# Performance work log

Measured on AMD Instinct MI355X. Metric: run time of the kernel, lower is better.

Reference implementation:

```python
import jax, jax.numpy as jnp
import numpy as np
import math

D_MODEL = 512
D_STATE = 16
D_CONV = 4
EXPAND = 2
D_INNER = EXPAND * D_MODEL          # 1024
D_HALF = D_INNER // 2               # 512
DT_RANK = math.ceil(D_MODEL / 16)   # 32
BATCH, SEQLEN = 2, 4096
DT_MIN, DT_MAX, DT_FLOOR = 0.001, 0.1, 1e-4


def setup_inputs() -> dict:
    key = jax.random.key(0)
    ks = jax.random.split(key, 9)

    def lin(k, fan_out, fan_in):
        return jax.random.normal(k, (fan_out, fan_in), jnp.float32) / np.float32(np.sqrt(fan_in))

    hidden_states = jax.random.normal(ks[0], (BATCH, SEQLEN, D_MODEL), jnp.float32)
    in_proj_w = lin(ks[1], D_INNER, D_MODEL)
    x_proj_w = lin(ks[2], DT_RANK + 2 * D_STATE, D_HALF)
    dt_std = np.float32(DT_RANK ** -0.5)
    dt_proj_w = jax.random.uniform(ks[3], (D_HALF, DT_RANK), jnp.float32, -dt_std, dt_std)
    dt = jnp.exp(jax.random.uniform(ks[4], (D_HALF,), jnp.float32)
                 * (math.log(DT_MAX) - math.log(DT_MIN)) + math.log(DT_MIN))
    dt = jnp.clip(dt, DT_FLOOR)
    dt_proj_b = dt + jnp.log(-jnp.expm1(-dt))  # inverse-softplus init
    A_log = jnp.log(jnp.tile(jnp.arange(1, D_STATE + 1, dtype=jnp.float32)[None, :], (D_HALF, 1)))
    D = jnp.ones((D_HALF,), jnp.float32)
    out_proj_w = lin(ks[5], D_MODEL, D_INNER)
    conv1d_x_w = jax.random.normal(ks[6], (D_HALF, 1, D_CONV), jnp.float32) / np.float32(np.sqrt(D_CONV))
    conv1d_z_w = jax.random.normal(ks[7], (D_HALF, 1, D_CONV), jnp.float32) / np.float32(np.sqrt(D_CONV))
    return dict(hidden_states=hidden_states, in_proj_w=in_proj_w,
                conv1d_x_w=conv1d_x_w, conv1d_z_w=conv1d_z_w,
                x_proj_w=x_proj_w, dt_proj_w=dt_proj_w, dt_proj_b=dt_proj_b,
                A_log=A_log, D=D, out_proj_w=out_proj_w)


def _dwconv_same(x, w):
    # x: (b, c, l); w: (c, 1, k) depthwise. torch padding='same' with k=4 pads (1, 2),
    # which matches lax 'SAME'.
    return jax.lax.conv_general_dilated(
        x, w, window_strides=(1,), padding='SAME',
        dimension_numbers=('NCH', 'OIH', 'NCH'),
        feature_group_count=x.shape[1])


def _selective_scan(x, delta, A, B, C, D):
    # x, delta: (b, d, l); A: (d, n); B, C: (b, n, l); D: (d,)
    dA = jnp.exp(jnp.einsum('bdl,dn->bldn', delta, A))        # (b, l, d, n)
    dBx = jnp.einsum('bdl,bnl,bdl->bldn', delta, B, x)        # (b, l, d, n)

    def combine(c1, c2):
        a1, b1 = c1
        a2, b2 = c2
        return a1 * a2, a2 * b1 + b2

    _, h = jax.lax.associative_scan(combine, (dA, dBx), axis=1)  # h: (b, l, d, n)
    y = jnp.einsum('bldn,bnl->bdl', h, C) + D[None, :, None] * x
    return y


def reference(hidden_states, in_proj_w, conv1d_x_w, conv1d_z_w, x_proj_w,
              dt_proj_w, dt_proj_b, A_log, D, out_proj_w):
    b, l, _ = hidden_states.shape
    xz = jnp.einsum('bld,ed->bel', hidden_states, in_proj_w)   # (b, d_inner, l)
    x, z = jnp.split(xz, 2, axis=1)                            # each (b, d_half, l)
    A = -jnp.exp(A_log.astype(jnp.float32))
    x = jax.nn.silu(_dwconv_same(x, conv1d_x_w))
    z = jax.nn.silu(_dwconv_same(z, conv1d_z_w))
    x_dbl = jnp.einsum('bdl,ed->bel', x, x_proj_w)             # (b, dt_rank+2n, l)
    dt_r = x_dbl[:, :DT_RANK]                                  # (b, dt_rank, l)
    Bm = x_dbl[:, DT_RANK:DT_RANK + D_STATE]                   # (b, n, l)
    Cm = x_dbl[:, DT_RANK + D_STATE:]                          # (b, n, l)
    dt = jnp.einsum('brl,dr->bdl', dt_r, dt_proj_w)            # (b, d_half, l)
    delta = jax.nn.softplus(dt + dt_proj_b.astype(jnp.float32)[None, :, None])
    y = _selective_scan(x, delta, A, Bm, Cm, D.astype(jnp.float32))
    y = jnp.concatenate([y, z], axis=1)                        # (b, d_inner, l)
    out = jnp.einsum('bdl,ed->ble', y, out_proj_w)             # (b, l, d_model)
    return out
```

## Files before the change

kernel.cpp:

```cpp
#include <hip/hip_runtime.h>
#include <math.h>

#define BB 2
#define LL 4096
#define DMODEL 512
#define DINNER 1024
#define DHALF 512
#define DSTATE 16
#define RK 32
#define NCH 64
#define NC 128
#define CLEN (LL/NC)
#define NG 16
#define GL (NC/NG)

typedef __attribute__((ext_vector_type(8))) short short8;
typedef __attribute__((ext_vector_type(4))) float f32x4;

__device__ __forceinline__ float silu_f(float v) { return v / (1.f + __expf(-v)); }

__device__ __forceinline__ unsigned short f2bf(float x) {
    unsigned int u = __float_as_uint(x);
    u += 0x7fffu + ((u >> 16) & 1u);
    return (unsigned short)(u >> 16);
}
__device__ __forceinline__ float bf2f(unsigned short u) {
    return __uint_as_float((unsigned int)u << 16);
}

__device__ __forceinline__ float softplus_f(float x) {
    return fmaxf(x, 0.f) + __logf(1.f + __expf(-fabsf(x)));
}

__device__ __forceinline__ void gload16(const unsigned short* g, unsigned short* l) {
    __builtin_amdgcn_global_load_lds((const __attribute__((address_space(1))) void*)g,
                                     (__attribute__((address_space(3))) void*)l, 16, 0, 0);
}

#define H4  1048576
#define W14 131072
#define W24 131072
#define W34 8192
__global__ void cast_all(const float* __restrict__ hid, const float* __restrict__ w1,
                         const float* __restrict__ w2, const float* __restrict__ w3,
                         unsigned short* __restrict__ Hb, unsigned short* __restrict__ Wb,
                         unsigned short* __restrict__ Wob, unsigned short* __restrict__ Wxb) {
    int i = blockIdx.x * 256 + threadIdx.x;
    const float* src; unsigned short* dst; int j;
    if (i < H4)                    { src = hid; dst = Hb;  j = i; }
    else if (i < H4 + W14)         { src = w1;  dst = Wb;  j = i - H4; }
    else if (i < H4 + W14 + W24)   { src = w2;  dst = Wob; j = i - H4 - W14; }
    else if (i < H4 + W14 + W24 + W34) { src = w3; dst = Wxb; j = i - H4 - W14 - W24; }
    else return;
    float4 v = *(const float4*)&src[(size_t)j * 4];
    ushort4 o = make_ushort4(f2bf(v.x), f2bf(v.y), f2bf(v.z), f2bf(v.w));
    *(ushort4*)&dst[(size_t)j * 4] = o;
}

template<int K, int E, bool BF16OUT>
__global__ __launch_bounds__(256) void gemm_mfma(const unsigned short* __restrict__ W,
                                                 const unsigned short* __restrict__ X,
                                                 void* __restrict__ outv) {
    __shared__ unsigned short Wa[128 * 64];
    __shared__ unsigned short Xa[128 * 64];
    const int tid = threadIdx.x;
    const int lane = tid & 63;
    const int w = tid >> 6;
    const int wr = w >> 1, wc = w & 1;
    const int frow = lane & 15;
    const int kg = lane >> 4;
    const int e0 = blockIdx.y * 128;
    const int r0 = blockIdx.x * 128;

    f32x4 acc[4][4] = {};

    for (int kt = 0; kt < K / 64; ++kt) {
        #pragma unroll
        for (int i = 0; i < 4; ++i) {
            int flat = i * 256 + tid;
            int row = flat >> 3;
            int slot = flat & 7;
            int chunk = slot ^ (row & 7);
            gload16(&W[(size_t)(e0 + row) * K + kt * 64 + chunk * 8], &Wa[flat * 8]);
            gload16(&X[(size_t)(r0 + row) * K + kt * 64 + chunk * 8], &Xa[flat * 8]);
        }
        __syncthreads();

        #pragma unroll
        for (int ks = 0; ks < 2; ++ks) {
            short8 af[4], bfr[4];
            #pragma unroll
            for (int m = 0; m < 4; ++m) {
                int row = wr * 64 + m * 16 + frow;
                int phys = (ks * 4 + kg) ^ (row & 7);
                af[m] = *(const short8*)&Wa[row * 64 + phys * 8];
            }
            #pragma unroll
            for (int n = 0; n < 4; ++n) {
                int row = wc * 64 + n * 16 + frow;
                int phys = (ks * 4 + kg) ^ (row & 7);
                bfr[n] = *(const short8*)&Xa[row * 64 + phys * 8];
            }
            #pragma unroll
            for (int m = 0; m < 4; ++m)
                #pragma unroll
                for (int n = 0; n < 4; ++n)
                    acc[m][n] = __builtin_amdgcn_mfma_f32_16x16x32_bf16(af[m], bfr[n], acc[m][n], 0, 0, 0);
        }
        __syncthreads();
    }

    #pragma unroll
    for (int m = 0; m < 4; ++m) {
        #pragma unroll
        for (int n = 0; n < 4; ++n) {
            int e = e0 + wr * 64 + m * 16 + kg * 4;
            int r = r0 + wc * 64 + n * 16 + frow;
            f32x4 a = acc[m][n];
            if constexpr (BF16OUT) {
                ushort4 o = make_ushort4(f2bf(a.x), f2bf(a.y), f2bf(a.z), f2bf(a.w));
                *(ushort4*)&((unsigned short*)outv)[(size_t)r * E + e] = o;
            } else {
                *(f32x4*)&((float*)outv)[(size_t)r * E + e] = a;
            }
        }
    }
}

__global__ __launch_bounds__(256) void gemm_xproj(const unsigned short* __restrict__ W,
                                                  const unsigned short* __restrict__ X,
                                                  float* __restrict__ out) {
    __shared__ unsigned short Xa[128 * 64];
    __shared__ unsigned short Wa[64 * 64];
    const int tid = threadIdx.x;
    const int lane = tid & 63;
    const int w = tid >> 6;
    const int frow = lane & 15;
    const int kg = lane >> 4;
    const int r0 = blockIdx.x * 128;

    f32x4 acc[4][2] = {};

    for (int kt = 0; kt < 512 / 64; ++kt) {
        #pragma unroll
        for (int i = 0; i < 4; ++i) {
            int flat = i * 256 + tid;
            int row = flat >> 3;
            int slot = flat & 7;
            int chunk = slot ^ (row & 7);
            gload16(&X[(size_t)(r0 + row) * 512 + kt * 64 + chunk * 8], &Xa[flat * 8]);
        }
        #pragma unroll
        for (int i = 0; i < 2; ++i) {
            int flat = i * 256 + tid;
            int row = flat >> 3;
            int slot = flat & 7;
            int chunk = slot ^ (row & 7);
            gload16(&W[(size_t)row * 512 + kt * 64 + chunk * 8], &Wa[flat * 8]);
        }
        __syncthreads();

        #pragma unroll
        for (int ks = 0; ks < 2; ++ks) {
            short8 af[4], bfr[2];
            #pragma unroll
            for (int m = 0; m < 4; ++m) {
                int row = m * 16 + frow;
                int phys = (ks * 4 + kg) ^ (row & 7);
                af[m] = *(const short8*)&Wa[row * 64 + phys * 8];
            }
            #pragma unroll
            for (int n = 0; n < 2; ++n) {
                int row = w * 32 + n * 16 + frow;
                int phys = (ks * 4 + kg) ^ (row & 7);
                bfr[n] = *(const short8*)&Xa[row * 64 + phys * 8];
            }
            #pragma unroll
            for (int m = 0; m < 4; ++m)
                #pragma unroll
                for (int n = 0; n < 2; ++n)
                    acc[m][n] = __builtin_amdgcn_mfma_f32_16x16x32_bf16(af[m], bfr[n], acc[m][n], 0, 0, 0);
        }
        __syncthreads();
    }

    #pragma unroll
    for (int m = 0; m < 4; ++m) {
        #pragma unroll
        for (int n = 0; n < 2; ++n) {
            int r = r0 + w * 32 + n * 16 + frow;
            int b = r >> 12;
            int l = r & (LL - 1);
            int e = m * 16 + kg * 4;
            #pragma unroll
            for (int i = 0; i < 4; ++i)
                out[((size_t)b * NCH + e + i) * LL + l] = acc[m][n][i];
        }
    }
}

__global__ void conv_silu(const unsigned short* __restrict__ xzb,
                          const float* __restrict__ wx, const float* __restrict__ wz,
                          unsigned short* __restrict__ xqb, unsigned short* __restrict__ ycb) {
    __shared__ float s[67][64];
    const int b = blockIdx.z;
    const int l0 = blockIdx.x * 64;
    const int c0 = blockIdx.y * 64;
    const int tid = threadIdx.x;
    for (int idx = tid; idx < 67 * 16; idx += 256) {
        int rr = idx >> 4, u = idx & 15;
        int l = l0 - 1 + rr;
        float4 f;
        if (l >= 0 && l < LL) {
            ushort4 v = *(const ushort4*)&xzb[((size_t)b * LL + l) * DINNER + c0 + u * 4];
            f = make_float4(bf2f(v.x), bf2f(v.y), bf2f(v.z), bf2f(v.w));
        } else f = make_float4(0.f, 0.f, 0.f, 0.f);
        *(float4*)&s[rr][u * 4] = f;
    }
    __syncthreads();
    const int ct = (tid & 15) * 4;
    const int c = c0 + ct;
    const bool isx = (c < DHALF);
    const float* wp = isx ? &wx[c * 4] : &wz[(c - DHALF) * 4];
    float4 w0 = *(const float4*)&wp[0];
    float4 w1 = *(const float4*)&wp[4];
    float4 w2 = *(const float4*)&wp[8];
    float4 w3 = *(const float4*)&wp[12];
    #pragma unroll
    for (int rep = 0; rep < 4; ++rep) {
        int ll = (tid >> 4) + rep * 16;
        float4 t0 = *(const float4*)&s[ll][ct];
        float4 t1 = *(const float4*)&s[ll + 1][ct];
        float4 t2 = *(const float4*)&s[ll + 2][ct];
        float4 t3 = *(const float4*)&s[ll + 3][ct];
        float v0 = w0.x*t0.x + w0.y*t1.x + w0.z*t2.x + w0.w*t3.x;
        float v1 = w1.x*t0.y + w1.y*t1.y + w1.z*t2.y + w1.w*t3.y;
        float v2 = w2.x*t0.z + w2.y*t1.z + w2.z*t2.z + w2.w*t3.z;
        float v3 = w3.x*t0.w + w3.y*t1.w + w3.z*t2.w + w3.w*t3.w;
        ushort4 o = make_ushort4(f2bf(silu_f(v0)), f2bf(silu_f(v1)),
                                 f2bf(silu_f(v2)), f2bf(silu_f(v3)));
        int l = l0 + ll;
        if (isx) *(ushort4*)&xqb[((size_t)b * LL + l) * DHALF + c] = o;
        else     *(ushort4*)&ycb[((size_t)b * LL + l) * DINNER + c] = o;
    }
}

__global__ __launch_bounds__(256) void scan1(const unsigned short* __restrict__ xqb,
                      const float* __restrict__ xdbl, const float* __restrict__ A_log,
                      const float* __restrict__ dtw, const float* __restrict__ dtb,
                      float* __restrict__ pend, float* __restrict__ hend) {
    __shared__ float s[48][CLEN];
    const int b = blockIdx.z;
    const int d = blockIdx.y * 256 + threadIdx.x;
    const int c = blockIdx.x;
    const int tid = threadIdx.x;
    for (int idx = tid; idx < 48 * CLEN; idx += 256) {
        int ch = idx / CLEN, ll = idx % CLEN;
        s[ch][ll] = xdbl[((size_t)b * NCH + ch) * LL + c * CLEN + ll];
    }
    float dtwreg[RK];
    #pragma unroll
    for (int r = 0; r < RK; r += 4) {
        float4 v = *(const float4*)&dtw[d * RK + r];
        dtwreg[r] = v.x; dtwreg[r+1] = v.y; dtwreg[r+2] = v.z; dtwreg[r+3] = v.w;
    }
    float Arow[DSTATE];
    #pragma unroll
    for (int n = 0; n < DSTATE; ++n) Arow[n] = -expf(A_log[d * DSTATE + n]);
    const float bias = dtb[d];
    float del[CLEN];
    #pragma unroll
    for (int t = 0; t < CLEN; ++t) del[t] = bias;
    __syncthreads();
    #pragma unroll
    for (int r = 0; r < RK; ++r) {
        float wv = dtwreg[r];
        #pragma unroll
        for (int q = 0; q < CLEN / 4; ++q) {
            float4 v = *(const float4*)&s[r][q * 4];
            del[q*4+0] = fmaf(v.x, wv, del[q*4+0]);
            del[q*4+1] = fmaf(v.y, wv, del[q*4+1]);
            del[q*4+2] = fmaf(v.z, wv, del[q*4+2]);
            del[q*4+3] = fmaf(v.w, wv, del[q*4+3]);
        }
    }
    #pragma unroll
    for (int t = 0; t < CLEN; ++t) del[t] = softplus_f(del[t]);

    float h[DSTATE], p[DSTATE];
    #pragma unroll
    for (int n = 0; n < DSTATE; ++n) { h[n] = 0.f; p[n] = 1.f; }
    #pragma unroll
    for (int t = 0; t < CLEN; ++t) {
        float dl = del[t];
        float xv = bf2f(xqb[((size_t)b * LL + c * CLEN + t) * DHALF + d]);
        float dx = dl * xv;
        #pragma unroll
        for (int n = 0; n < DSTATE; ++n) {
            float dA = __expf(dl * Arow[n]);
            h[n] = fmaf(dA, h[n], dx * s[32 + n][t]);
            p[n] *= dA;
        }
    }
    size_t base = (((size_t)b * NC + c) * DSTATE) * DHALF + d;
    #pragma unroll
    for (int n = 0; n < DSTATE; ++n) {
        pend[base + (size_t)n * DHALF] = p[n];
        hend[base + (size_t)n * DHALF] = h[n];
    }
}

__global__ void scan2a(float* __restrict__ pend, float* __restrict__ hend,
                       float* __restrict__ gP, float* __restrict__ gH) {
    int flat = blockIdx.x * 256 + threadIdx.x;
    int d = flat & (DHALF - 1);
    int n = (flat >> 9) & (DSTATE - 1);
    int g = (flat >> 13) & (NG - 1);
    int b = flat >> 17;
    const size_t stride = (size_t)DSTATE * DHALF;
    size_t idx = (((size_t)b * NC + g * GL) * DSTATE + n) * DHALF + d;
    float P = 1.f, H = 0.f;
    #pragma unroll
    for (int j = 0; j < GL; ++j) {
        float p = pend[idx], h = hend[idx];
        pend[idx] = P; hend[idx] = H;
        H = fmaf(p, H, h);
        P *= p;
        idx += stride;
    }
    size_t gi = (((size_t)b * NG + g) * DSTATE + n) * DHALF + d;
    gP[gi] = P; gH[gi] = H;
}

__global__ void scan2b(const float* __restrict__ gP, float* __restrict__ gH) {
    int flat = blockIdx.x * 256 + threadIdx.x;
    int d = flat & (DHALF - 1);
    int n = (flat >> 9) & (DSTATE - 1);
    int b = flat >> 13;
    float h = 0.f;
    const size_t stride = (size_t)DSTATE * DHALF;
    size_t gi = (((size_t)b * NG) * DSTATE + n) * DHALF + d;
    for (int g = 0; g < NG; ++g) {
        float P = gP[gi], Hh = gH[gi];
        gH[gi] = h;
        h = fmaf(P, h, Hh);
        gi += stride;
    }
}

__global__ __launch_bounds__(256) void scan3(const unsigned short* __restrict__ xqb,
                      const float* __restrict__ xdbl, const float* __restrict__ A_log,
                      const float* __restrict__ dtw, const float* __restrict__ dtb,
                      const float* __restrict__ Dp, const float* __restrict__ pend,
                      const float* __restrict__ hend, const float* __restrict__ gH,
                      unsigned short* __restrict__ ycb) {
    __shared__ float s[64][CLEN];
    const int b = blockIdx.z;
    const int d = blockIdx.y * 256 + threadIdx.x;
    const int c = blockIdx.x;
    const int tid = threadIdx.x;
    for (int idx = tid; idx < 64 * CLEN; idx += 256) {
        int ch = idx / CLEN, ll = idx % CLEN;
        s[ch][ll] = xdbl[((size_t)b * NCH + ch) * LL + c * CLEN + ll];
    }
    float dtwreg[RK];
    #pragma unroll
    for (int r = 0; r < RK; r += 4) {
        float4 v = *(const float4*)&dtw[d * RK + r];
        dtwreg[r] = v.x; dtwreg[r+1] = v.y; dtwreg[r+2] = v.z; dtwreg[r+3] = v.w;
    }
    float Arow[DSTATE], h[DSTATE];
    size_t base = (((size_t)b * NC + c) * DSTATE) * DHALF + d;
    size_t gbase = (((size_t)b * NG + (c / GL)) * DSTATE) * DHALF + d;
    #pragma unroll
    for (int n = 0; n < DSTATE; ++n) {
        Arow[n] = -expf(A_log[d * DSTATE + n]);
        h[n] = fmaf(pend[base + (size_t)n * DHALF], gH[gbase + (size_t)n * DHALF],
                    hend[base + (size_t)n * DHALF]);
    }
    const float bias = dtb[d];
    const float Dv = Dp[d];
    float del[CLEN];
    #pragma unroll
    for (int t = 0; t < CLEN; ++t) del[t] = bias;
    __syncthreads();
    #pragma unroll
    for (int r = 0; r < RK; ++r) {
        float wv = dtwreg[r];
        #pragma unroll
        for (int q = 0; q < CLEN / 4; ++q) {
            float4 v = *(const float4*)&s[r][q * 4];
            del[q*4+0] = fmaf(v.x, wv, del[q*4+0]);
            del[q*4+1] = fmaf(v.y, wv, del[q*4+1]);
            del[q*4+2] = fmaf(v.z, wv, del[q*4+2]);
            del[q*4+3] = fmaf(v.w, wv, del[q*4+3]);
        }
    }
    #pragma unroll
    for (int t = 0; t < CLEN; ++t) del[t] = softplus_f(del[t]);

    #pragma unroll
    for (int t = 0; t < CLEN; ++t) {
        float dl = del[t];
        float xv = bf2f(xqb[((size_t)b * LL + c * CLEN + t) * DHALF + d]);
        float dx = dl * xv;
        float y = Dv * xv;
        #pragma unroll
        for (int n = 0; n < DSTATE; ++n) {
            float dA = __expf(dl * Arow[n]);
            h[n] = fmaf(dA, h[n], dx * s[32 + n][t]);
            y = fmaf(h[n], s[48 + n][t], y);
        }
        ycb[((size_t)b * LL + c * CLEN + t) * DINNER + d] = f2bf(y);
    }
}

extern "C" void kernel_launch(void* const* d_in, const int* in_sizes, int n_in,
                              void* d_out, int out_size, void* d_ws, size_t ws_size,
                              hipStream_t stream) {
    const float* hidden     = (const float*)d_in[0];
    const float* in_proj_w  = (const float*)d_in[1];
    const float* conv_x_w   = (const float*)d_in[2];
    const float* conv_z_w   = (const float*)d_in[3];
    const float* x_proj_w   = (const float*)d_in[4];
    const float* dt_proj_w  = (const float*)d_in[5];
    const float* dt_proj_b  = (const float*)d_in[6];
    const float* A_log      = (const float*)d_in[7];
    const float* Dp         = (const float*)d_in[8];
    const float* out_proj_w = (const float*)d_in[9];
    float* out = (float*)d_out;

    float* ws_f = (float*)d_ws;
    unsigned short* Wb  = (unsigned short*)(ws_f + 0);
    unsigned short* Wob = (unsigned short*)(ws_f + 262144);
    unsigned short* Wxb = (unsigned short*)(ws_f + 524288);
    unsigned short* Hb  = (unsigned short*)(ws_f + 540672);
    unsigned short* xzb = (unsigned short*)(ws_f + 2637824);
    unsigned short* xqb = (unsigned short*)(ws_f + 6832128);
    unsigned short* ycb = (unsigned short*)(ws_f + 8929280);
    float* xdbl = ws_f + 13123584;
    float* gP   = ws_f + 13647872;
    float* gH   = ws_f + 13910016;
    float* pend = ws_f + 2637824;
    float* hend = ws_f + 540672;

    dim3 blk(256);

    cast_all<<<dim3((H4 + W14 + W24 + W34 + 255) / 256), blk, 0, stream>>>(
        hidden, in_proj_w, out_proj_w, x_proj_w, Hb, Wb, Wob, Wxb);
    gemm_mfma<DMODEL, DINNER, true><<<dim3(BB * LL / 128, DINNER / 128), blk, 0, stream>>>(Wb, Hb, xzb);
    conv_silu<<<dim3(LL / 64, DINNER / 64, BB), blk, 0, stream>>>(xzb, conv_x_w, conv_z_w, xqb, ycb);
    gemm_xproj<<<dim3(BB * LL / 128), blk, 0, stream>>>(Wxb, xqb, xdbl);
    scan1<<<dim3(NC, DHALF / 256, BB), blk, 0, stream>>>(xqb, xdbl, A_log, dt_proj_w, dt_proj_b, pend, hend);
    scan2a<<<dim3(BB * NG * DSTATE * DHALF / 256), blk, 0, stream>>>(pend, hend, gP, gH);
    scan2b<<<dim3(BB * DSTATE * DHALF / 256), blk, 0, stream>>>(gP, gH);
    scan3<<<dim3(NC, DHALF / 256, BB), blk, 0, stream>>>(xqb, xdbl, A_log, dt_proj_w, dt_proj_b,
                                                         Dp, pend, hend, gH, ycb);
    gemm_mfma<DINNER, DMODEL, false><<<dim3(BB * LL / 128, DMODEL / 128), blk, 0, stream>>>(Wob, ycb, out);
}
```

Baseline: 134.8 us.

## Use exp2 with prescaled A, closed-form chunk decay, and XCD-aware GEMM tile remap

The scan kernels now fold log2(e) into A so each decay factor is a single exp2 instead of exp with an extra multiply. The first scan pass no longer multiplies a running product per state; it sums the deltas and computes the chunk decay once as exp2(A*sum(delta)). The GEMM kernel remaps block IDs so consecutive blocks on the same XCD share weight tiles, which targets L2 locality. The closed-form product changes rounding slightly, and the remap assumes gridDim.x is divisible by 8.

Measured after the change: 157.5 us. 16.9% more time.

```diff
diff --git a/kernel.cpp b/kernel.cpp
--- a/kernel.cpp
+++ b/kernel.cpp
@@ -13,6 +13,7 @@
 #define CLEN (LL/NC)
 #define NG 16
 #define GL (NC/NG)
+#define LOG2E 1.44269504088896f
 
 typedef __attribute__((ext_vector_type(8))) short short8;
 typedef __attribute__((ext_vector_type(4))) float f32x4;
@@ -69,8 +70,16 @@
     const int wr = w >> 1, wc = w & 1;
     const int frow = lane & 15;
     const int kg = lane >> 4;
-    const int e0 = blockIdx.y * 128;
-    const int r0 = blockIdx.x * 128;
+
+    const int bid = blockIdx.y * gridDim.x + blockIdx.x;
+    const int GY = gridDim.y;
+    const int nxs = gridDim.x >> 3;
+    const int xcd = bid & 7;
+    const int idx = bid >> 3;
+    const int bx = xcd * nxs + idx / GY;
+    const int by = idx % GY;
+    const int e0 = by * 128;
+    const int r0 = bx * 128;
 
     f32x4 acc[4][4] = {};
 
@@ -264,9 +273,9 @@
         float4 v = *(const float4*)&dtw[d * RK + r];
         dtwreg[r] = v.x; dtwreg[r+1] = v.y; dtwreg[r+2] = v.z; dtwreg[r+3] = v.w;
     }
-    float Arow[DSTATE];
-    #pragma unroll
-    for (int n = 0; n < DSTATE; ++n) Arow[n] = -expf(A_log[d * DSTATE + n]);
+    float Arow2[DSTATE];
+    #pragma unroll
+    for (int n = 0; n < DSTATE; ++n) Arow2[n] = -expf(A_log[d * DSTATE + n]) * LOG2E;
     const float bias = dtb[d];
     float del[CLEN];
     #pragma unroll
@@ -284,12 +293,13 @@
             del[q*4+3] = fmaf(v.w, wv, del[q*4+3]);
         }
     }
-    #pragma unroll
-    for (int t = 0; t < CLEN; ++t) del[t] = softplus_f(del[t]);
-
-    float h[DSTATE], p[DSTATE];
-    #pragma unroll
-    for (int n = 0; n < DSTATE; ++n) { h[n] = 0.f; p[n] = 1.f; }
+    float sdel = 0.f;
+    #pragma unroll
+    for (int t = 0; t < CLEN; ++t) { del[t] = softplus_f(del[t]); sdel += del[t]; }
+
+    float h[DSTATE];
+    #pragma unroll
+    for (int n = 0; n < DSTATE; ++n) h[n] = 0.f;
     #pragma unroll
     for (int t = 0; t < CLEN; ++t) {
         float dl = del[t];
@@ -297,15 +307,14 @@
         float dx = dl * xv;
         #pragma unroll
         for (int n = 0; n < DSTATE; ++n) {
-            float dA = __expf(dl * Arow[n]);
+            float dA = exp2f(dl * Arow2[n]);
             h[n] = fmaf(dA, h[n], dx * s[32 + n][t]);
-            p[n] *= dA;
         }
     }
     size_t base = (((size_t)b * NC + c) * DSTATE) * DHALF + d;
     #pragma unroll
     for (int n = 0; n < DSTATE; ++n) {
-        pend[base + (size_t)n * DHALF] = p[n];
+        pend[base + (size_t)n * DHALF] = exp2f(Arow2[n] * sdel);
         hend[base + (size_t)n * DHALF] = h[n];
     }
 }
@@ -369,12 +378,12 @@
         float4 v = *(const float4*)&dtw[d * RK + r];
         dtwreg[r] = v.x; dtwreg[r+1] = v.y; dtwreg[r+2] = v.z; dtwreg[r+3] = v.w;
     }
-    float Arow[DSTATE], h[DSTATE];
+    float Arow2[DSTATE], h[DSTATE];
     size_t base = (((size_t)b * NC + c) * DSTATE) * DHALF + d;
     size_t gbase = (((size_t)b * NG + (c / GL)) * DSTATE) * DHALF + d;
     #pragma unroll
     for (int n = 0; n < DSTATE; ++n) {
-        Arow[n] = -expf(A_log[d * DSTATE + n]);
+        Arow2[n] = -expf(A_log[d * DSTATE + n]) * LOG2E;
         h[n] = fmaf(pend[base + (size_t)n * DHALF], gH[gbase + (size_t)n * DHALF],
                     hend[base + (size_t)n * DHALF]);
     }
@@ -407,7 +416,7 @@
         float y = Dv * xv;
         #pragma unroll
         for (int n = 0; n < DSTATE; ++n) {
-            float dA = __expf(dl * Arow[n]);
+            float dA = exp2f(dl * Arow2[n]);
             h[n] = fmaf(dA, h[n], dx * s[32 + n][t]);
             y = fmaf(h[n], s[48 + n][t], y);
         }
```
